# Performance work log

Measured on AMD Instinct MI355X. Metric: run time of the kernel, lower is better.

The kernel has to match this reference:

```python
import jax, jax.numpy as jnp
import numpy as np
from jax import lax

B, S, T = 256, 2048, 64


def setup_inputs() -> dict:
    key = jax.random.key(0)
    k1, k2, k3 = jax.random.split(key, 3)
    emissions = jax.random.normal(k1, (B, S, T), dtype=jnp.float32)
    tags = jax.random.randint(k2, (B, S), 0, T, dtype=jnp.int64)
    mask = jnp.ones((B, S), dtype=bool)
    # learned parameter: transitions ~ U(-0.1, 0.1) per reset_parameters
    transitions = jax.random.uniform(k3, (T, T), dtype=jnp.float32, minval=-0.1, maxval=0.1)
    return {"emissions": emissions, "transitions": transitions, "tags": tags, "mask": mask}


def _crf_nll(emissions, transitions, tags, mask):
    # emissions [B,S,T], tags [B,S] int, mask [B,S] bool -> scalar NLL
    em = jnp.swapaxes(emissions, 0, 1)        # [S,B,T]
    tg = jnp.swapaxes(tags, 0, 1)             # [S,B]
    mk = jnp.swapaxes(mask, 0, 1)             # [S,B]
    bsz = tg.shape[1]
    batch_range = jnp.arange(bsz)

    # ---- score(emissions, tags, mask): fully vectorized over seq ----
    em_at_tags = jnp.take_along_axis(em, tg[..., None], axis=-1)[..., 0]   # [S,B]
    trans_steps = transitions[tg[:-1], tg[1:]]                              # [S-1,B]
    step_scores = (trans_steps + em_at_tags[1:]) * mk[1:].astype(em.dtype)  # [S-1,B]
    gold_score = em[0, batch_range, tg[0]] + jnp.sum(step_scores, axis=0)   # [B]

    # ---- normalization: logsumexp semiring scan over seq ----
    def step(score, inp):
        e_t, m_t = inp                                   # [B,T], [B]
        # score[b, i] + transitions[i, j] + e_t[b, j] -> lse over i
        s_ = jax.nn.logsumexp(score[:, :, None] + transitions[None] + e_t[:, None, :], axis=1)
        score = jnp.where(m_t[:, None], s_, score)
        return score, None

    final, _ = lax.scan(step, em[0], (em[1:], mk[1:]))
    log_z = jax.nn.logsumexp(final, axis=-1)             # [B]

    return -jnp.mean(gold_score - log_z)


def reference(emissions, transitions, tags, mask):
    return _crf_nll(emissions, transitions, tags, mask)
```

## Files before the change

### kernel.cpp

```cpp
#include <hip/hip_runtime.h>
#include <cstdint>

#define BB 256
#define SS 2048
#define TT 64
#define LOG64 4.158883083359672

#define OUTB 0
#define GBASE 256
#define LBASE 512
#define PBASE 8704
#define WS_NEED ((size_t)(PBASE + 2048 * 4096) * 4)
#define SEGL 256

#define M_SPLIT 1024
#define WS_STRIDE 144

typedef short  s16x4  __attribute__((ext_vector_type(4)));
typedef float  f32x4v __attribute__((ext_vector_type(4)));
typedef unsigned int u32x2 __attribute__((ext_vector_type(2)));

#if __has_builtin(__builtin_amdgcn_mfma_f32_16x16x16bf16_1k)
#define HAVE_MFMA16 1
#define MFMA16(A,B,C) __builtin_amdgcn_mfma_f32_16x16x16bf16_1k(A,B,C,0,0,0)
#else
#define HAVE_MFMA16 0
#endif

__device__ __forceinline__ int ldtag(const uint32_t* tw, int i, int is64) {
    return (int)tw[i << is64];
}

__device__ __forceinline__ unsigned pk_rne(float lo, float hi) {
    unsigned ul = __float_as_uint(lo) + 0x8000u;
    unsigned uh = __float_as_uint(hi) + 0x8000u;
    return __builtin_amdgcn_perm(uh, ul, 0x07060302u);
}

#if HAVE_MFMA16
__global__ __launch_bounds__(64, 4) void crf_seg_kernel(
    const float* __restrict__ em, const float* __restrict__ trans,
    float* __restrict__ ws)
{
    const int l = threadIdx.x;
    const int idx = blockIdx.x;
    const int b = idx >> 5, s = (idx >> 2) & 7, w = idx & 3;
    const int l15 = l & 15, l4 = l >> 4;
    __shared__ __align__(16) float f_lds[TT];

#define EV(mt,kb,e) (__expf(trans[((kb)*16 + l4*4 + (e))*64 + (mt)*16 + l15]) * 0.015625f)
#define MKA(NM,mt,kb) u32x2 NM##u; NM##u[0]=pk_rne(EV(mt,kb,0),EV(mt,kb,1)); \
                      NM##u[1]=pk_rne(EV(mt,kb,2),EV(mt,kb,3)); \
                      const s16x4 NM=__builtin_bit_cast(s16x4,NM##u);
    MKA(A00,0,0) MKA(A01,0,1) MKA(A02,0,2) MKA(A03,0,3)
    MKA(A10,1,0) MKA(A11,1,1) MKA(A12,1,2) MKA(A13,1,3)
    MKA(A20,2,0) MKA(A21,2,1) MKA(A22,2,2) MKA(A23,2,3)
    MKA(A30,3,0) MKA(A31,3,1) MKA(A32,3,2) MKA(A33,3,3)
#undef MKA
#undef EV

    const int cn = w * 16 + l15;
    u32x2 B0u, B1u, B2u, B3u;
#define BINIT(Bu,kb) { float v0=((kb)*16+l4*4+0)==cn?1.f:0.f; \
                       float v1=((kb)*16+l4*4+1)==cn?1.f:0.f; \
                       float v2=((kb)*16+l4*4+2)==cn?1.f:0.f; \
                       float v3=((kb)*16+l4*4+3)==cn?1.f:0.f; \
                       Bu[0]=pk_rne(v0,v1); Bu[1]=pk_rne(v2,v3); }
    BINIT(B0u,0) BINIT(B1u,1) BINIT(B2u,2) BINIT(B3u,3)
#undef BINIT

    const size_t ebase = (size_t)b * (SS * TT);
    const int t0 = s * SEGL + 1;
    const int t1 = (s == 7) ? (SS - 1) : (s + 1) * SEGL;
    const int nst = t1 - t0 + 1;

    float p0 = em[ebase + (size_t)(t0 + 0) * TT + l];
    float p1 = em[ebase + (size_t)(t0 + 1) * TT + l];
    float p2 = em[ebase + (size_t)(t0 + 2) * TT + l];
    float p3 = em[ebase + (size_t)(t0 + 3) * TT + l];

    float logacc = 0.f;
    const f32x4v Zf = {0.f, 0.f, 0.f, 0.f};
    f32x4v C0, C1, C2, C3;

    for (int si = 0; si < nst; ++si) {
        const float fr = __expf(p0);
        p0 = p1; p1 = p2; p2 = p3;
        int tp = t0 + si + 4; if (tp > SS - 1) tp = SS - 1;
        p3 = em[ebase + (size_t)tp * TT + l];

        f_lds[l] = fr;

        const s16x4 Bf0 = __builtin_bit_cast(s16x4, B0u);
        const s16x4 Bf1 = __builtin_bit_cast(s16x4, B1u);
        const s16x4 Bf2 = __builtin_bit_cast(s16x4, B2u);
        const s16x4 Bf3 = __builtin_bit_cast(s16x4, B3u);

        C0 = MFMA16(A00,Bf0,Zf); C0 = MFMA16(A01,Bf1,C0); C0 = MFMA16(A02,Bf2,C0); C0 = MFMA16(A03,Bf3,C0);
        C1 = MFMA16(A10,Bf0,Zf); C1 = MFMA16(A11,Bf1,C1); C1 = MFMA16(A12,Bf2,C1); C1 = MFMA16(A13,Bf3,C1);
        C2 = MFMA16(A20,Bf0,Zf); C2 = MFMA16(A21,Bf1,C2); C2 = MFMA16(A22,Bf2,C2); C2 = MFMA16(A23,Bf3,C2);
        C3 = MFMA16(A30,Bf0,Zf); C3 = MFMA16(A31,Bf1,C3); C3 = MFMA16(A32,Bf2,C3); C3 = MFMA16(A33,Bf3,C3);

        const f32x4v fm0 = *(const f32x4v*)(f_lds +  0 + l4 * 4);
        const f32x4v fm1 = *(const f32x4v*)(f_lds + 16 + l4 * 4);
        const f32x4v fm2 = *(const f32x4v*)(f_lds + 32 + l4 * 4);
        const f32x4v fm3 = *(const f32x4v*)(f_lds + 48 + l4 * 4);
        C0 *= fm0; C1 *= fm1; C2 *= fm2; C3 *= fm3;

        if ((si & 7) == 7) {
            float mx = fmaxf(fmaxf(fmaxf(C0[0],C0[1]),fmaxf(C0[2],C0[3])),
                       fmaxf(fmaxf(fmaxf(C1[0],C1[1]),fmaxf(C1[2],C1[3])),
                       fmaxf(fmaxf(fmaxf(C2[0],C2[1]),fmaxf(C2[2],C2[3])),
                             fmaxf(fmaxf(C3[0],C3[1]),fmaxf(C3[2],C3[3])))));
            mx = fmaxf(mx, __shfl_xor(mx, 1));  mx = fmaxf(mx, __shfl_xor(mx, 2));
            mx = fmaxf(mx, __shfl_xor(mx, 4));  mx = fmaxf(mx, __shfl_xor(mx, 8));
            mx = fmaxf(mx, __shfl_xor(mx, 16)); mx = fmaxf(mx, __shfl_xor(mx, 32));
            const float inv = __builtin_amdgcn_rcpf(mx);
            C0 *= inv; C1 *= inv; C2 *= inv; C3 *= inv;
            logacc += __logf(mx);
        }

        B0u[0] = pk_rne(C0[0],C0[1]); B0u[1] = pk_rne(C0[2],C0[3]);
        B1u[0] = pk_rne(C1[0],C1[1]); B1u[1] = pk_rne(C1[2],C1[3]);
        B2u[0] = pk_rne(C2[0],C2[1]); B2u[1] = pk_rne(C2[2],C2[3]);
        B3u[0] = pk_rne(C3[0],C3[1]); B3u[1] = pk_rne(C3[2],C3[3]);
    }

    float* pt = ws + PBASE + (size_t)(b * 8 + s) * 4096 + (size_t)cn * 64 + l4 * 4;
    *(f32x4v*)(pt +  0) = C0;
    *(f32x4v*)(pt + 16) = C1;
    *(f32x4v*)(pt + 32) = C2;
    *(f32x4v*)(pt + 48) = C3;
    if (l == 0)
        ws[LBASE + (b * 8 + s) * 4 + w] = logacc + (float)((double)nst * LOG64);
}

__global__ __launch_bounds__(64) void crf_combine2(
    const float* __restrict__ em, float* __restrict__ ws)
{
    const int b = blockIdx.x, m = threadIdx.x;
    __shared__ float xs[TT];
    float alpha = __expf(em[(size_t)b * (SS * TT) + m]);
    float logA = 0.f;
    for (int s = 0; s < 8; ++s) {
        const float* Lp = ws + LBASE + (b * 8 + s) * 4;
        const float L0 = Lp[0], L1 = Lp[1], L2 = Lp[2], L3 = Lp[3];
        const float Lmax = fmaxf(fmaxf(L0, L1), fmaxf(L2, L3));
        const float Lw = Lp[m >> 4];
        xs[m] = alpha * __expf(Lw - Lmax);
        const float* Pp = ws + PBASE + (size_t)(b * 8 + s) * 4096;
        float y = 0.f;
        for (int i = 0; i < TT; ++i)
            y = fmaf(Pp[(size_t)i * 64 + m], xs[i], y);
        logA += Lmax;
        float mx = y;
        mx = fmaxf(mx, __shfl_xor(mx, 1));  mx = fmaxf(mx, __shfl_xor(mx, 2));
        mx = fmaxf(mx, __shfl_xor(mx, 4));  mx = fmaxf(mx, __shfl_xor(mx, 8));
        mx = fmaxf(mx, __shfl_xor(mx, 16)); mx = fmaxf(mx, __shfl_xor(mx, 32));
        alpha = y * __builtin_amdgcn_rcpf(mx);
        logA += __logf(mx);
    }
    float ssum = alpha;
    ssum += __shfl_xor(ssum, 1);  ssum += __shfl_xor(ssum, 2);
    ssum += __shfl_xor(ssum, 4);  ssum += __shfl_xor(ssum, 8);
    ssum += __shfl_xor(ssum, 16); ssum += __shfl_xor(ssum, 32);
    if (m == 0)
        ws[OUTB + b] = ws[GBASE + b] - (logA + __logf(ssum));
}
#endif

__global__ __launch_bounds__(256) void crf_gold_kernel(
    const float* __restrict__ em, const float* __restrict__ trans,
    const uint32_t* __restrict__ tw, float* __restrict__ gdst, int gstride)
{
    const int b = blockIdx.x, tid = threadIdx.x;
    uint32_t orv = 0;
    for (int k = 1; k < 32; k += 2) orv |= tw[k];
    const int is64 = (orv == 0) ? 1 : 0;
    const int    tbase = b * SS;
    const size_t ebase = (size_t)b * SS * TT;
    float s = 0.0f;
    for (int t = tid; t < SS; t += 256) {
        const int tg = ldtag(tw, tbase + t, is64);
        float v = em[ebase + (size_t)t * TT + tg];
        if (t > 0) {
            const int tp = ldtag(tw, tbase + t - 1, is64);
            v += trans[tp * TT + tg];
        }
        s += v;
    }
    for (int off = 1; off < 64; off <<= 1) s += __shfl_xor(s, off);
    __shared__ float sh[4];
    if ((tid & 63) == 0) sh[tid >> 6] = s;
    __syncthreads();
    if (tid == 0) gdst[b * gstride] = sh[0] + sh[1] + sh[2] + sh[3];
}

__device__ __forceinline__ float qsum4(float v) {
    int a = __builtin_amdgcn_mov_dpp(__float_as_int(v), 0xB1, 0xF, 0xF, true);
    float v1 = v + __int_as_float(a);
    int b2 = __builtin_amdgcn_mov_dpp(__float_as_int(v1), 0x4E, 0xF, 0xF, true);
    return v1 + __int_as_float(b2);
}
#define LDS_BARRIER() asm volatile("s_waitcnt lgkmcnt(0)\n\ts_barrier" ::: "memory")

template <int DIR>
__device__ __forceinline__ void fb_run(const float* __restrict__ em,
                                       const float* __restrict__ trans,
                                       float* __restrict__ ws,
                                       float* __restrict__ qbuf,
                                       int b, int tid)
{
    const int l   = tid & 63;
    const int w   = tid >> 6;
    const int j   = (w << 4) | (l >> 2);
    const int sub = l & 3;
#define TRIDX(k) (DIR ? (j * 64 + (sub * 16 + (k))) : ((sub * 16 + (k)) * 64 + j))
#define ED(k) const float E##k = __expf(trans[TRIDX(k)]) * 0.015625f;
    ED(0) ED(1) ED(2) ED(3) ED(4) ED(5) ED(6) ED(7)
    ED(8) ED(9) ED(10) ED(11) ED(12) ED(13) ED(14) ED(15)
#undef ED
#undef TRIDX
    const size_t ebase  = (size_t)b * SS * TT;
    constexpr int nsteps = DIR ? (SS - M_SPLIT) : (M_SPLIT - 1);
    constexpr int estep  = DIR ? -TT : TT;
    constexpr int t0     = DIR ? (SS - 2) : 1;
    const float* ep = em + ebase + (size_t)t0 * TT + j;
    float p0 = ep[0];
    float p1 = ep[1 * estep];
    float p2 = ep[2 * estep];
    float p3 = ep[3 * estep];
    if (tid < TT) {
        const size_t it = DIR ? ((size_t)(SS - 1) * TT) : 0;
        qbuf[tid] = __expf(em[ebase + it + tid]);
    }
    LDS_BARRIER();
    float logsum = 0.0f;
    int cur = 0;
    for (int si = 0; si < nsteps; ++si) {
        const float e = p0;
        p0 = p1; p1 = p2; p2 = p3;
        p3 = ep[4 * estep];
        ep += estep;
        float* rb = qbuf + (cur << 6);
        float* wb = qbuf + ((cur ^ 1) << 6);
        const float4 q0 = *(const float4*)(rb + sub * 16 + 0);
        const float4 q1 = *(const float4*)(rb + sub * 16 + 4);
        const float4 q2 = *(const float4*)(rb + sub * 16 + 8);
        const float4 q3 = *(const float4*)(rb + sub * 16 + 12);
        float a0 = 0, a1 = 0, a2 = 0, a3 = 0;
        a0 = fmaf(q0.x, E0,  a0); a1 = fmaf(q0.y, E1,  a1);
        a2 = fmaf(q0.z, E2,  a2); a3 = fmaf(q0.w, E3,  a3);
        a0 = fmaf(q1.x, E4,  a0); a1 = fmaf(q1.y, E5,  a1);
        a2 = fmaf(q1.z, E6,  a2); a3 = fmaf(q1.w, E7,  a3);
        a0 = fmaf(q2.x, E8,  a0); a1 = fmaf(q2.y, E9,  a1);
        a2 = fmaf(q2.z, E10, a2); a3 = fmaf(q2.w, E11, a3);
        a0 = fmaf(q3.x, E12, a0); a1 = fmaf(q3.y, E13, a1);
        a2 = fmaf(q3.z, E14, a2); a3 = fmaf(q3.w, E15, a3);
        float dot = (a0 + a1) + (a2 + a3);
        dot = qsum4(dot);
        float fv = __expf(e);
        if (DIR && si == nsteps - 1) fv = 1.0f;
        float wval = dot * fv;
        if ((si & 63) == 63) {
            const float m = rb[0];
            wval *= __builtin_amdgcn_rcpf(m);
            if (tid == 0) logsum += __logf(m);
        }
        if (sub == 0) wb[j] = wval;
        LDS_BARRIER();
        cur ^= 1;
    }
    const float* fin = qbuf + (cur << 6);
    float* wsb = ws + (size_t)b * WS_STRIDE;
    if (tid < TT) wsb[(DIR ? TT : 0) + tid] = fin[tid];
    if (tid == 0) wsb[DIR ? 129 : 128] = (float)((double)nsteps * LOG64) + logsum;
}

__global__ __launch_bounds__(256) void crf_fb_kernel(
    const float* __restrict__ em, const float* __restrict__ trans,
    float* __restrict__ ws)
{
    const int b   = blockIdx.x & (BB - 1);
    const int dir = blockIdx.x >> 8;
    __shared__ __align__(16) float qbuf[2 * TT];
    if (dir == 0) fb_run<0>(em, trans, ws, qbuf, b, threadIdx.x);
    else          fb_run<1>(em, trans, ws, qbuf, b, threadIdx.x);
}

__global__ __launch_bounds__(64) void crf_combine_kernel(
    const float* __restrict__ ws, float* __restrict__ outb)
{
    const int b = blockIdx.x, lane = threadIdx.x;
    const float* wsb = ws + (size_t)b * WS_STRIDE;
    float p = wsb[lane] * wsb[64 + lane];
    for (int off = 1; off < 64; off <<= 1) p += __shfl_xor(p, off);
    if (lane == 0) {
        const float logz = wsb[128] + wsb[129] + __logf(p);
        outb[b] = wsb[130] - logz;
    }
}

__global__ __launch_bounds__(256) void crf_final_kernel(
    const float* __restrict__ vals, float* __restrict__ out)
{
    const int l = threadIdx.x;
    float v = vals[l];
    for (int off = 1; off < 64; off <<= 1) v += __shfl_xor(v, off);
    __shared__ float sh[4];
    if ((l & 63) == 0) sh[l >> 6] = v;
    __syncthreads();
    if (l == 0) out[0] = -(sh[0] + sh[1] + sh[2] + sh[3]) * (1.0f / BB);
}

extern "C" void kernel_launch(void* const* d_in, const int* in_sizes, int n_in,
                              void* d_out, int out_size, void* d_ws, size_t ws_size,
                              hipStream_t stream) {
    const float*    em    = (const float*)d_in[0];
    const float*    trans = (const float*)d_in[1];
    const uint32_t* tw    = (const uint32_t*)d_in[2];
    float* ws = (float*)d_ws;

#if HAVE_MFMA16
    if (ws_size >= WS_NEED) {
        crf_seg_kernel<<<BB * 32, 64, 0, stream>>>(em, trans, ws);
        crf_gold_kernel<<<BB, 256, 0, stream>>>(em, trans, tw, ws + GBASE, 1);
        crf_combine2<<<BB, 64, 0, stream>>>(em, ws);
        crf_final_kernel<<<1, 256, 0, stream>>>(ws + OUTB, (float*)d_out);
        return;
    }
#endif
    float* outb = ws + (size_t)BB * WS_STRIDE;
    crf_fb_kernel<<<2 * BB, 256, 0, stream>>>(em, trans, ws);
    crf_gold_kernel<<<BB, 256, 0, stream>>>(em, trans, tw, ws + 130, WS_STRIDE);
    crf_combine_kernel<<<BB, 64, 0, stream>>>(ws, outb);
    crf_final_kernel<<<1, 256, 0, stream>>>(outb, (float*)d_out);
}
```

Measured before the change: 296.7 us.

## Use hardware bf16 packing, per-column rescaling and bf16 segment matrices

Replaces the manual add-and-permute bf16 rounding with the v_cvt_pk_bf16_f32 instruction in the segment kernel's recurrence. The periodic renormalisation now takes a max over each output column instead of the whole wave, which needs two shuffles instead of six. This is valid because each column propagates independently, and each column now keeps its own log-scale. Segment transfer matrices are stored in bf16 and the combine kernel widens them back, halving that workspace traffic. The segment count is chosen from the workspace size, which adds some precision risk from storing P in bf16.

After: 414.9 us. 39.8% more time.

```diff
diff --git a/kernel.cpp b/kernel.cpp
--- a/kernel.cpp
+++ b/kernel.cpp
@@ -9,9 +9,8 @@
 #define OUTB 0
 #define GBASE 256
 #define LBASE 512
-#define PBASE 8704
-#define WS_NEED ((size_t)(PBASE + 2048 * 4096) * 4)
-#define SEGL 256
+#define LSIZE (256 * 8 * 64)
+#define PBASE_F (LBASE + LSIZE)
 
 #define M_SPLIT 1024
 #define WS_STRIDE 144
@@ -20,38 +19,43 @@
 typedef float  f32x4v __attribute__((ext_vector_type(4)));
 typedef unsigned int u32x2 __attribute__((ext_vector_type(2)));
 
-#if __has_builtin(__builtin_amdgcn_mfma_f32_16x16x16bf16_1k)
-#define HAVE_MFMA16 1
-#define MFMA16(A,B,C) __builtin_amdgcn_mfma_f32_16x16x16bf16_1k(A,B,C,0,0,0)
-#else
-#define HAVE_MFMA16 0
-#endif
-
 __device__ __forceinline__ int ldtag(const uint32_t* tw, int i, int is64) {
     return (int)tw[i << is64];
 }
 
-__device__ __forceinline__ unsigned pk_rne(float lo, float hi) {
-    unsigned ul = __float_as_uint(lo) + 0x8000u;
-    unsigned uh = __float_as_uint(hi) + 0x8000u;
-    return __builtin_amdgcn_perm(uh, ul, 0x07060302u);
-}
-
-#if HAVE_MFMA16
+__device__ __forceinline__ unsigned cvt_pk_bf16(float lo, float hi) {
+    unsigned r;
+    asm("v_cvt_pk_bf16_f32 %0, %1, %2" : "=v"(r) : "v"(lo), "v"(hi));
+    return r;
+}
+
+__device__ __forceinline__ f32x4v mfma16(u32x2 a, u32x2 b, f32x4v c) {
+#if __has_builtin(__builtin_amdgcn_mfma_f32_16x16x16bf16_1k)
+    return __builtin_amdgcn_mfma_f32_16x16x16bf16_1k(
+        __builtin_bit_cast(s16x4, a), __builtin_bit_cast(s16x4, b), c, 0, 0, 0);
+#else
+    f32x4v d;
+    asm("v_mfma_f32_16x16x16_bf16 %0, %1, %2, %3"
+        : "=v"(d) : "v"(a), "v"(b), "v"(c));
+    return d;
+#endif
+}
+
 __global__ __launch_bounds__(64, 4) void crf_seg_kernel(
     const float* __restrict__ em, const float* __restrict__ trans,
-    float* __restrict__ ws)
+    float* __restrict__ ws, int sshift)
 {
     const int l = threadIdx.x;
-    const int idx = blockIdx.x;
-    const int b = idx >> 5, s = (idx >> 2) & 7, w = idx & 3;
+    const int nseg = 1 << sshift;
+    const int b = blockIdx.x >> sshift;
+    const int s = blockIdx.x & (nseg - 1);
+    const int w = blockIdx.y;
     const int l15 = l & 15, l4 = l >> 4;
     __shared__ __align__(16) float f_lds[TT];
 
 #define EV(mt,kb,e) (__expf(trans[((kb)*16 + l4*4 + (e))*64 + (mt)*16 + l15]) * 0.015625f)
-#define MKA(NM,mt,kb) u32x2 NM##u; NM##u[0]=pk_rne(EV(mt,kb,0),EV(mt,kb,1)); \
-                      NM##u[1]=pk_rne(EV(mt,kb,2),EV(mt,kb,3)); \
-                      const s16x4 NM=__builtin_bit_cast(s16x4,NM##u);
+#define MKA(NM,mt,kb) u32x2 NM; NM[0]=cvt_pk_bf16(EV(mt,kb,0),EV(mt,kb,1)); \
+                      NM[1]=cvt_pk_bf16(EV(mt,kb,2),EV(mt,kb,3));
     MKA(A00,0,0) MKA(A01,0,1) MKA(A02,0,2) MKA(A03,0,3)
     MKA(A10,1,0) MKA(A11,1,1) MKA(A12,1,2) MKA(A13,1,3)
     MKA(A20,2,0) MKA(A21,2,1) MKA(A22,2,2) MKA(A23,2,3)
@@ -65,13 +69,14 @@
                        float v1=((kb)*16+l4*4+1)==cn?1.f:0.f; \
                        float v2=((kb)*16+l4*4+2)==cn?1.f:0.f; \
                        float v3=((kb)*16+l4*4+3)==cn?1.f:0.f; \
-                       Bu[0]=pk_rne(v0,v1); Bu[1]=pk_rne(v2,v3); }
+                       Bu[0]=cvt_pk_bf16(v0,v1); Bu[1]=cvt_pk_bf16(v2,v3); }
     BINIT(B0u,0) BINIT(B1u,1) BINIT(B2u,2) BINIT(B3u,3)
 #undef BINIT
 
     const size_t ebase = (size_t)b * (SS * TT);
-    const int t0 = s * SEGL + 1;
-    const int t1 = (s == 7) ? (SS - 1) : (s + 1) * SEGL;
+    const int L  = SS >> sshift;
+    const int t0 = s * L + 1;
+    const int t1 = (s == nseg - 1) ? (SS - 1) : (s + 1) * L;
     const int nst = t1 - t0 + 1;
 
     float p0 = em[ebase + (size_t)(t0 + 0) * TT + l];
@@ -91,83 +96,80 @@
 
         f_lds[l] = fr;
 
-        const s16x4 Bf0 = __builtin_bit_cast(s16x4, B0u);
-        const s16x4 Bf1 = __builtin_bit_cast(s16x4, B1u);
-        const s16x4 Bf2 = __builtin_bit_cast(s16x4, B2u);
-        const s16x4 Bf3 = __builtin_bit_cast(s16x4, B3u);
-
-        C0 = MFMA16(A00,Bf0,Zf); C0 = MFMA16(A01,Bf1,C0); C0 = MFMA16(A02,Bf2,C0); C0 = MFMA16(A03,Bf3,C0);
-        C1 = MFMA16(A10,Bf0,Zf); C1 = MFMA16(A11,Bf1,C1); C1 = MFMA16(A12,Bf2,C1); C1 = MFMA16(A13,Bf3,C1);
-        C2 = MFMA16(A20,Bf0,Zf); C2 = MFMA16(A21,Bf1,C2); C2 = MFMA16(A22,Bf2,C2); C2 = MFMA16(A23,Bf3,C2);
-        C3 = MFMA16(A30,Bf0,Zf); C3 = MFMA16(A31,Bf1,C3); C3 = MFMA16(A32,Bf2,C3); C3 = MFMA16(A33,Bf3,C3);
-
-        const f32x4v fm0 = *(const f32x4v*)(f_lds +  0 + l4 * 4);
-        const f32x4v fm1 = *(const f32x4v*)(f_lds + 16 + l4 * 4);
-        const f32x4v fm2 = *(const f32x4v*)(f_lds + 32 + l4 * 4);
-        const f32x4v fm3 = *(const f32x4v*)(f_lds + 48 + l4 * 4);
-        C0 *= fm0; C1 *= fm1; C2 *= fm2; C3 *= fm3;
+        C0 = mfma16(A00,B0u,Zf); C0 = mfma16(A01,B1u,C0); C0 = mfma16(A02,B2u,C0); C0 = mfma16(A03,B3u,C0);
+        C1 = mfma16(A10,B0u,Zf); C1 = mfma16(A11,B1u,C1); C1 = mfma16(A12,B2u,C1); C1 = mfma16(A13,B3u,C1);
+        C2 = mfma16(A20,B0u,Zf); C2 = mfma16(A21,B1u,C2); C2 = mfma16(A22,B2u,C2); C2 = mfma16(A23,B3u,C2);
+        C3 = mfma16(A30,B0u,Zf); C3 = mfma16(A31,B1u,C3); C3 = mfma16(A32,B2u,C3); C3 = mfma16(A33,B3u,C3);
+
+        C0 *= *(const f32x4v*)(f_lds +  0 + l4 * 4);
+        C1 *= *(const f32x4v*)(f_lds + 16 + l4 * 4);
+        C2 *= *(const f32x4v*)(f_lds + 32 + l4 * 4);
+        C3 *= *(const f32x4v*)(f_lds + 48 + l4 * 4);
 
         if ((si & 7) == 7) {
             float mx = fmaxf(fmaxf(fmaxf(C0[0],C0[1]),fmaxf(C0[2],C0[3])),
                        fmaxf(fmaxf(fmaxf(C1[0],C1[1]),fmaxf(C1[2],C1[3])),
                        fmaxf(fmaxf(fmaxf(C2[0],C2[1]),fmaxf(C2[2],C2[3])),
                              fmaxf(fmaxf(C3[0],C3[1]),fmaxf(C3[2],C3[3])))));
-            mx = fmaxf(mx, __shfl_xor(mx, 1));  mx = fmaxf(mx, __shfl_xor(mx, 2));
-            mx = fmaxf(mx, __shfl_xor(mx, 4));  mx = fmaxf(mx, __shfl_xor(mx, 8));
-            mx = fmaxf(mx, __shfl_xor(mx, 16)); mx = fmaxf(mx, __shfl_xor(mx, 32));
+            mx = fmaxf(mx, __shfl_xor(mx, 16));
+            mx = fmaxf(mx, __shfl_xor(mx, 32));
             const float inv = __builtin_amdgcn_rcpf(mx);
             C0 *= inv; C1 *= inv; C2 *= inv; C3 *= inv;
             logacc += __logf(mx);
         }
 
-        B0u[0] = pk_rne(C0[0],C0[1]); B0u[1] = pk_rne(C0[2],C0[3]);
-        B1u[0] = pk_rne(C1[0],C1[1]); B1u[1] = pk_rne(C1[2],C1[3]);
-        B2u[0] = pk_rne(C2[0],C2[1]); B2u[1] = pk_rne(C2[2],C2[3]);
-        B3u[0] = pk_rne(C3[0],C3[1]); B3u[1] = pk_rne(C3[2],C3[3]);
-    }
-
-    float* pt = ws + PBASE + (size_t)(b * 8 + s) * 4096 + (size_t)cn * 64 + l4 * 4;
-    *(f32x4v*)(pt +  0) = C0;
-    *(f32x4v*)(pt + 16) = C1;
-    *(f32x4v*)(pt + 32) = C2;
-    *(f32x4v*)(pt + 48) = C3;
-    if (l == 0)
-        ws[LBASE + (b * 8 + s) * 4 + w] = logacc + (float)((double)nst * LOG64);
+        B0u[0] = cvt_pk_bf16(C0[0],C0[1]); B0u[1] = cvt_pk_bf16(C0[2],C0[3]);
+        B1u[0] = cvt_pk_bf16(C1[0],C1[1]); B1u[1] = cvt_pk_bf16(C1[2],C1[3]);
+        B2u[0] = cvt_pk_bf16(C2[0],C2[1]); B2u[1] = cvt_pk_bf16(C2[2],C2[3]);
+        B3u[0] = cvt_pk_bf16(C3[0],C3[1]); B3u[1] = cvt_pk_bf16(C3[2],C3[3]);
+    }
+
+    uint16_t* ptu = (uint16_t*)(ws + PBASE_F)
+                  + (size_t)blockIdx.x * 4096 + (size_t)cn * 64 + l4 * 4;
+    *(unsigned*)(ptu +  0) = cvt_pk_bf16(C0[0],C0[1]);
+    *(unsigned*)(ptu +  2) = cvt_pk_bf16(C0[2],C0[3]);
+    *(unsigned*)(ptu + 16) = cvt_pk_bf16(C1[0],C1[1]);
+    *(unsigned*)(ptu + 18) = cvt_pk_bf16(C1[2],C1[3]);
+    *(unsigned*)(ptu + 32) = cvt_pk_bf16(C2[0],C2[1]);
+    *(unsigned*)(ptu + 34) = cvt_pk_bf16(C2[2],C2[3]);
+    *(unsigned*)(ptu + 48) = cvt_pk_bf16(C3[0],C3[1]);
+    *(unsigned*)(ptu + 50) = cvt_pk_bf16(C3[2],C3[3]);
+    if (l4 == 0)
+        ws[LBASE + blockIdx.x * 64 + cn] = logacc + (float)((double)nst * LOG64);
 }
 
 __global__ __launch_bounds__(64) void crf_combine2(
-    const float* __restrict__ em, float* __restrict__ ws)
+    const float* __restrict__ em, float* __restrict__ ws, int sshift)
 {
     const int b = blockIdx.x, m = threadIdx.x;
+    const int nseg = 1 << sshift;
     __shared__ float xs[TT];
     float alpha = __expf(em[(size_t)b * (SS * TT) + m]);
     float logA = 0.f;
-    for (int s = 0; s < 8; ++s) {
-        const float* Lp = ws + LBASE + (b * 8 + s) * 4;
-        const float L0 = Lp[0], L1 = Lp[1], L2 = Lp[2], L3 = Lp[3];
-        const float Lmax = fmaxf(fmaxf(L0, L1), fmaxf(L2, L3));
-        const float Lw = Lp[m >> 4];
-        xs[m] = alpha * __expf(Lw - Lmax);
-        const float* Pp = ws + PBASE + (size_t)(b * 8 + s) * 4096;
+    for (int s = 0; s < nseg; ++s) {
+        const int seg = b * nseg + s;
+        const float Li = ws[LBASE + seg * 64 + m];
+        float Lmax = Li;
+        for (int off = 1; off < 64; off <<= 1) Lmax = fmaxf(Lmax, __shfl_xor(Lmax, off));
+        xs[m] = alpha * __expf(Li - Lmax);
+        const uint16_t* Pp = (const uint16_t*)(ws + PBASE_F) + (size_t)seg * 4096;
         float y = 0.f;
-        for (int i = 0; i < TT; ++i)
-            y = fmaf(Pp[(size_t)i * 64 + m], xs[i], y);
+#pragma unroll 8
+        for (int i = 0; i < TT; ++i) {
+            const float pv = __uint_as_float((unsigned)Pp[i * 64 + m] << 16);
+            y = fmaf(pv, xs[i], y);
+        }
         logA += Lmax;
         float mx = y;
-        mx = fmaxf(mx, __shfl_xor(mx, 1));  mx = fmaxf(mx, __shfl_xor(mx, 2));
-        mx = fmaxf(mx, __shfl_xor(mx, 4));  mx = fmaxf(mx, __shfl_xor(mx, 8));
-        mx = fmaxf(mx, __shfl_xor(mx, 16)); mx = fmaxf(mx, __shfl_xor(mx, 32));
+        for (int off = 1; off < 64; off <<= 1) mx = fmaxf(mx, __shfl_xor(mx, off));
         alpha = y * __builtin_amdgcn_rcpf(mx);
         logA += __logf(mx);
     }
     float ssum = alpha;
-    ssum += __shfl_xor(ssum, 1);  ssum += __shfl_xor(ssum, 2);
-    ssum += __shfl_xor(ssum, 4);  ssum += __shfl_xor(ssum, 8);
-    ssum += __shfl_xor(ssum, 16); ssum += __shfl_xor(ssum, 32);
+    for (int off = 1; off < 64; off <<= 1) ssum += __shfl_xor(ssum, off);
     if (m == 0)
         ws[OUTB + b] = ws[GBASE + b] - (logA + __logf(ssum));
 }
-#endif
 
 __global__ __launch_bounds__(256) void crf_gold_kernel(
     const float* __restrict__ em, const float* __restrict__ trans,
@@ -321,15 +323,21 @@
     const uint32_t* tw    = (const uint32_t*)d_in[2];
     float* ws = (float*)d_ws;
 
-#if HAVE_MFMA16
-    if (ws_size >= WS_NEED) {
-        crf_seg_kernel<<<BB * 32, 64, 0, stream>>>(em, trans, ws);
+    int sshift = 0;
+    const size_t hdr = (size_t)PBASE_F * 4;
+    if      (ws_size >= hdr + (((size_t)BB << 3) * 4096 * 2)) sshift = 3;
+    else if (ws_size >= hdr + (((size_t)BB << 2) * 4096 * 2)) sshift = 2;
+    else if (ws_size >= hdr + (((size_t)BB << 1) * 4096 * 2)) sshift = 1;
+
+    if (sshift) {
+        dim3 g(BB << sshift, 4);
+        crf_seg_kernel<<<g, 64, 0, stream>>>(em, trans, ws, sshift);
         crf_gold_kernel<<<BB, 256, 0, stream>>>(em, trans, tw, ws + GBASE, 1);
-        crf_combine2<<<BB, 64, 0, stream>>>(em, ws);
+        crf_combine2<<<BB, 64, 0, stream>>>(em, ws, sshift);
         crf_final_kernel<<<1, 256, 0, stream>>>(ws + OUTB, (float*)d_out);
         return;
     }
-#endif
+
     float* outb = ws + (size_t)BB * WS_STRIDE;
     crf_fb_kernel<<<2 * BB, 256, 0, stream>>>(em, trans, ws);
     crf_gold_kernel<<<BB, 256, 0, stream>>>(em, trans, tw, ws + 130, WS_STRIDE);
```
